# Optimization experiments

Hardware: AMD Instinct MI355X
Metric: run time of the kernel (lower is better)

Reference implementation:

```python
import jax, jax.numpy as jnp
import numpy as np

EPS = 1e-5

def _layer_norm(x, g, b):
    mu = jnp.mean(x, axis=-1, keepdims=True)
    var = jnp.mean(jnp.square(x - mu), axis=-1, keepdims=True)
    return (x - mu) * jax.lax.rsqrt(var + EPS) * g + b

def setup_inputs() -> dict:
    key = jax.random.key(0)
    ks = jax.random.split(key, 8)
    B, S, H, NH, FF = 2, 2048, 2048, 16, 8192
    x = jax.random.normal(ks[0], (B, S, H), dtype=jnp.float32)
    # causal mask: True = masked (matches masked_fill semantics)
    mask = jnp.triu(jnp.ones((S, S), dtype=bool), k=1)
    sc = 0.02
    wq = jax.random.normal(ks[1], (H, H), dtype=jnp.float32) * sc
    wk = jax.random.normal(ks[2], (H, H), dtype=jnp.float32) * sc
    wv = jax.random.normal(ks[3], (H, H), dtype=jnp.float32) * sc
    wo = jax.random.normal(ks[4], (H, H), dtype=jnp.float32) * sc
    w_in = jax.random.normal(ks[5], (H, FF), dtype=jnp.float32) * sc
    w_out = jax.random.normal(ks[6], (FF, H), dtype=jnp.float32) * sc
    ln1_g = jnp.ones((H,), jnp.float32); ln1_b = jnp.zeros((H,), jnp.float32)
    ln2_g = jnp.ones((H,), jnp.float32); ln2_b = jnp.zeros((H,), jnp.float32)
    return {"x": x, "mask": mask, "wq": wq, "wk": wk, "wv": wv, "wo": wo,
            "w_in": w_in, "w_out": w_out,
            "ln1_g": ln1_g, "ln1_b": ln1_b, "ln2_g": ln2_g, "ln2_b": ln2_b}

def reference(x, mask, wq, wk, wv, wo, w_in, w_out, ln1_g, ln1_b, ln2_g, ln2_b):
    B, S, H = x.shape
    NH = 16
    HD = H // NH
    scale = HD ** (-0.5)
    # attention with pre-norm
    xn = _layer_norm(x, ln1_g, ln1_b)
    q = (xn @ wq).reshape(B, S, NH, HD)
    k = (xn @ wk).reshape(B, S, NH, HD)
    v = (xn @ wv).reshape(B, S, NH, HD)
    scores = jnp.einsum('bqhd,bkhd->bhqk', q, k) * scale
    scores = jnp.where(mask[:S, :S], -jnp.inf, scores)
    attn = jax.nn.softmax(scores, axis=-1)
    out = jnp.einsum('bhqk,bkhd->bqhd', attn, v).reshape(B, S, H)
    h = x + out @ wo
    # FFN with pre-norm, tanh-approx GELU
    hn = _layer_norm(h, ln2_g, ln2_b)
    ff = jax.nn.gelu(hn @ w_in, approximate=True) @ w_out
    return h + ff
```

## Files before the change

### kernel.cpp

```cpp
#include <hip/hip_runtime.h>
#include <hip/hip_bf16.h>

#define B_ 2
#define S_ 2048
#define H_ 2048
#define NH_ 16
#define HD_ 128
#define FF_ 8192

typedef __attribute__((ext_vector_type(8))) short bf16x8;
typedef __attribute__((ext_vector_type(4))) float f32x4;

#define NEG_BIG (-1e30f)

#define GLL16(gp, lp)                                                                    \
  __builtin_amdgcn_global_load_lds((const __attribute__((address_space(1))) void*)(gp),  \
                                   (__attribute__((address_space(3))) void*)(lp), 16, 0, 0)

__device__ __forceinline__ float b2f(unsigned short u) {
  union { unsigned int i; float f; } c; c.i = ((unsigned int)u) << 16; return c.f;
}
__device__ __forceinline__ unsigned short f2b(float f) {
  unsigned int u = __float_as_uint(f);
  u += 0x7fffu + ((u >> 16) & 1u);
  return (unsigned short)(u >> 16);
}
__device__ __forceinline__ float ldf(const void* p, size_t i, int f32) {
  return f32 ? ((const float*)p)[i] : b2f(((const unsigned short*)p)[i]);
}
__device__ __forceinline__ void unpack8(uint4 r, float* f) {
  f[0] = b2f((unsigned short)(r.x & 0xffffu)); f[1] = b2f((unsigned short)(r.x >> 16));
  f[2] = b2f((unsigned short)(r.y & 0xffffu)); f[3] = b2f((unsigned short)(r.y >> 16));
  f[4] = b2f((unsigned short)(r.z & 0xffffu)); f[5] = b2f((unsigned short)(r.z >> 16));
  f[6] = b2f((unsigned short)(r.w & 0xffffu)); f[7] = b2f((unsigned short)(r.w >> 16));
}

__global__ void detect_k(const unsigned int* __restrict__ x, int* __restrict__ flagp) {
  if (threadIdx.x == 0) {
    int c = 0;
    for (int i = 0; i < 256; ++i) {
      unsigned int e = (x[i] >> 7) & 0xffu;
      c += (e >= 97u && e <= 130u) ? 1 : 0;
    }
    *flagp = (c < 128) ? 1 : 0;
  }
}

__global__ __launch_bounds__(256) void transpose_k(const void* __restrict__ in,
                                                   unsigned short* __restrict__ out,
                                                   int R, int C,
                                                   const int* __restrict__ flagp) {
  __shared__ unsigned short tile[32][33];
  int f32 = *flagp;
  int r0 = blockIdx.y * 32, c0 = blockIdx.x * 32;
  int tx = threadIdx.x & 31, ty = threadIdx.x >> 5;
#pragma unroll
  for (int p = 0; p < 4; ++p)
    tile[ty + p * 8][tx] = f2b(ldf(in, (size_t)(r0 + ty + p * 8) * C + c0 + tx, f32));
  __syncthreads();
#pragma unroll
  for (int p = 0; p < 4; ++p)
    out[(size_t)(c0 + ty + p * 8) * R + r0 + tx] = tile[tx][ty + p * 8];
}

__global__ __launch_bounds__(256) void v_transpose_k(const unsigned short* __restrict__ qkv,
                                                     unsigned short* __restrict__ VT) {
  __shared__ unsigned short tile[32][33];
  int bh = blockIdx.z;
  int b = bh >> 4, h = bh & 15;
  int s0 = blockIdx.x * 32, d0 = blockIdx.y * 32;
  int tx = threadIdx.x & 31, ty = threadIdx.x >> 5;
#pragma unroll
  for (int p = 0; p < 4; ++p) {
    int s = s0 + ty + p * 8;
    tile[ty + p * 8][tx] = qkv[(size_t)(b * S_ + s) * (3 * H_) + 2 * H_ + h * HD_ + d0 + tx];
  }
  __syncthreads();
#pragma unroll
  for (int p = 0; p < 4; ++p)
    VT[((size_t)bh * HD_ + d0 + ty + p * 8) * S_ + s0 + tx] = tile[tx][ty + p * 8];
}

__global__ __launch_bounds__(256) void ln_k(const void* __restrict__ x,
                                            const void* __restrict__ g,
                                            const void* __restrict__ b,
                                            unsigned short* __restrict__ y,
                                            const int* __restrict__ flagp, int in_mode) {
  __shared__ float red[2][4];
  int f32 = *flagp;
  int xf = in_mode ? f32 : 0;
  int row = blockIdx.x;
  int t = threadIdx.x;
  float v[8];
  size_t base = (size_t)row * H_ + t * 8;
  if (xf) {
    const float4* p = reinterpret_cast<const float4*>((const float*)x + base);
    float4 u0 = p[0], u1 = p[1];
    v[0] = u0.x; v[1] = u0.y; v[2] = u0.z; v[3] = u0.w;
    v[4] = u1.x; v[5] = u1.y; v[6] = u1.z; v[7] = u1.w;
  } else {
    unpack8(*reinterpret_cast<const uint4*>((const unsigned short*)x + base), v);
  }
  float s1 = 0.f, s2 = 0.f;
#pragma unroll
  for (int i = 0; i < 8; ++i) { s1 += v[i]; s2 += v[i] * v[i]; }
#pragma unroll
  for (int off = 32; off > 0; off >>= 1) {
    s1 += __shfl_down(s1, off);
    s2 += __shfl_down(s2, off);
  }
  int w = t >> 6, lane = t & 63;
  if (lane == 0) { red[0][w] = s1; red[1][w] = s2; }
  __syncthreads();
  s1 = red[0][0] + red[0][1] + red[0][2] + red[0][3];
  s2 = red[1][0] + red[1][1] + red[1][2] + red[1][3];
  float mu = s1 * (1.0f / H_);
  float var = s2 * (1.0f / H_) - mu * mu;
  float rinv = rsqrtf(var + 1e-5f);
  float gv[8], bv[8];
#pragma unroll
  for (int i = 0; i < 8; ++i) {
    gv[i] = ldf(g, t * 8 + i, f32);
    bv[i] = ldf(b, t * 8 + i, f32);
  }
  unsigned int o[4];
#pragma unroll
  for (int i = 0; i < 4; ++i) {
    unsigned short lo = f2b((v[2 * i] - mu) * rinv * gv[2 * i] + bv[2 * i]);
    unsigned short hi = f2b((v[2 * i + 1] - mu) * rinv * gv[2 * i + 1] + bv[2 * i + 1]);
    o[i] = (unsigned int)lo | ((unsigned int)hi << 16);
  }
  uint4 ov; ov.x = o[0]; ov.y = o[1]; ov.z = o[2]; ov.w = o[3];
  *reinterpret_cast<uint4*>(y + base) = ov;
}

#define PH_BAR() do { asm volatile("" ::: "memory"); __builtin_amdgcn_s_barrier(); \
                      asm volatile("" ::: "memory"); } while (0)
#define VMC(n) asm volatile("s_waitcnt vmcnt(" #n ")" ::: "memory")

#define STA(buf_, h_, kt_) do {                                                        \
  GLL16(pA0 + (size_t)(h_) * 128 * K + (kt_) * 64, &LdsA[buf_][(h_) * 8192 + lw]);     \
  GLL16(pA1 + (size_t)(h_) * 128 * K + (kt_) * 64, &LdsA[buf_][(h_) * 8192 + 4096 + lw]); } while (0)
#define STB(buf_, h_, kt_) do {                                                        \
  GLL16(pB0 + (size_t)(h_) * 128 * K + (kt_) * 64, &LdsB[buf_][(h_) * 8192 + lw]);     \
  GLL16(pB1 + (size_t)(h_) * 128 * K + (kt_) * 64, &LdsB[buf_][(h_) * 8192 + 4096 + lw]); } while (0)

#define LDA4(AF, buf_, mb_) do { _Pragma("unroll")                                     \
  for (int mi_ = 0; mi_ < 4; ++mi_) {                                                  \
    const unsigned short* _p = &LdsA[buf_][(wr * 128 + ((mb_) + mi_) * 16 + l15) * 64];\
    AF[mi_][0] = *reinterpret_cast<const bf16x8*>(_p + cs0);                           \
    AF[mi_][1] = *reinterpret_cast<const bf16x8*>(_p + cs1); } } while (0)
#define LDB2(BF, buf_, nb_) do { _Pragma("unroll")                                     \
  for (int ni_ = 0; ni_ < 2; ++ni_) {                                                  \
    const unsigned short* _p = &LdsB[buf_][(wc * 64 + ((nb_) + ni_) * 16 + l15) * 64]; \
    BF[ni_][0] = *reinterpret_cast<const bf16x8*>(_p + cs0);                           \
    BF[ni_][1] = *reinterpret_cast<const bf16x8*>(_p + cs1); } } while (0)

#define MF8(AF, BF, MO, NO) do { _Pragma("unroll")                                     \
  for (int mi_ = 0; mi_ < 4; ++mi_) { _Pragma("unroll")                                \
    for (int ni_ = 0; ni_ < 2; ++ni_) {                                                \
      acc[(MO) + mi_][(NO) + ni_] = __builtin_amdgcn_mfma_f32_16x16x32_bf16(           \
          AF[mi_][0], BF[ni_][0], acc[(MO) + mi_][(NO) + ni_], 0, 0, 0);               \
      acc[(MO) + mi_][(NO) + ni_] = __builtin_amdgcn_mfma_f32_16x16x32_bf16(           \
          AF[mi_][1], BF[ni_][1], acc[(MO) + mi_][(NO) + ni_], 0, 0, 0);               \
    } } } while (0)

#define GITER(LAST, tO, tE2, tO2) do {                                                 \
                                                                              \
  LDA4(aL, 0, 0); LDB2(bL, 0, 0);                                                      \
  STA(1, 1, tO);                                                                       \
  PH_BAR(); __builtin_amdgcn_s_setprio(1);                                             \
  MF8(aL, bL, 0, 0);                                                                   \
  __builtin_amdgcn_s_setprio(0);                                                       \
                                                                              \
  LDB2(bH, 0, 2);                                                                      \
  PH_BAR(); __builtin_amdgcn_s_setprio(1);                                             \
  MF8(aL, bH, 0, 2);                                                                   \
  __builtin_amdgcn_s_setprio(0);                                                       \
                                                                              \
  LDA4(aH, 0, 4);                                                                      \
  if (!(LAST)) STB(0, 0, tE2);                                                         \
  PH_BAR(); __builtin_amdgcn_s_setprio(1);                                             \
  MF8(aH, bL, 4, 0);                                                                   \
  __builtin_amdgcn_s_setprio(0);                                                       \
                                                                              \
  if (!(LAST)) { STB(0, 1, tE2); STA(0, 0, tE2); VMC(6); } else { VMC(0); }            \
  PH_BAR(); __builtin_amdgcn_s_setprio(1);                                             \
  MF8(aH, bH, 4, 2);                                                                   \
  __builtin_amdgcn_s_setprio(0);                                                       \
                                                                              \
  LDA4(aL, 1, 0); LDB2(bL, 1, 0);                                                      \
  if (!(LAST)) STA(0, 1, tE2);                                                         \
  PH_BAR(); __builtin_amdgcn_s_setprio(1);                                             \
  MF8(aL, bL, 0, 0);                                                                   \
  __builtin_amdgcn_s_setprio(0);                                                       \
                                                                              \
  LDB2(bH, 1, 2);                                                                      \
  PH_BAR(); __builtin_amdgcn_s_setprio(1);                                             \
  MF8(aL, bH, 0, 2);                                                                   \
  __builtin_amdgcn_s_setprio(0);                                                       \
                                                                              \
  LDA4(aH, 1, 4);                                                                      \
  if (!(LAST)) STB(1, 0, tO2);                                                         \
  PH_BAR(); __builtin_amdgcn_s_setprio(1);                                             \
  MF8(aH, bL, 4, 0);                                                                   \
  __builtin_amdgcn_s_setprio(0);                                                       \
                                                                              \
  if (!(LAST)) { STB(1, 1, tO2); STA(1, 0, tO2); VMC(6); }                             \
  PH_BAR(); __builtin_amdgcn_s_setprio(1);                                             \
  MF8(aH, bH, 4, 2);                                                                   \
  __builtin_amdgcn_s_setprio(0);                                                       \
} while (0)

template <int EPI>
__global__ __launch_bounds__(512) void gemm256(const unsigned short* __restrict__ A,
                                               const unsigned short* __restrict__ BT,
                                               void* __restrict__ C,
                                               const void* __restrict__ resid,
                                               int M, int N, int K,
                                               const int* __restrict__ flagp,
                                               int resid_mode, int store_mode, int nbx,
                                               int nxy, int Klen,
                                               size_t pslice, int prow) {
  (void)M;
  __shared__ unsigned short LdsA[2][16384];
  __shared__ unsigned short LdsB[2][16384];

  unsigned nwg = gridDim.x, q = nwg >> 3;
  unsigned o = blockIdx.x;
  unsigned wg = (o & 7u) * q + (o >> 3);
  int ks = 0;
  if (nxy) { ks = (int)(wg / (unsigned)nxy); wg -= (unsigned)ks * (unsigned)nxy; }
  int bx = (int)(wg % (unsigned)nbx), by = (int)(wg / (unsigned)nbx);
  int m_base = by * 256, n_base = bx * 256;
  size_t koff = (size_t)ks * (size_t)Klen;

  int tid = threadIdx.x;
  int w = tid >> 6, lane = tid & 63;
  int l15 = lane & 15, quad = lane >> 4;
  int wr = w >> 2, wc = w & 3;

  int row0 = w * 8 + (lane >> 3);
  int scb  = (lane & 7) ^ (lane >> 3);
  const unsigned short* pA0 = A + (size_t)(m_base + row0) * K + koff + scb * 8;
  const unsigned short* pA1 = pA0 + (size_t)64 * K;
  const unsigned short* pB0 = BT + (size_t)(n_base + row0) * K + koff + scb * 8;
  const unsigned short* pB1 = pB0 + (size_t)64 * K;
  unsigned lw = (unsigned)w * 512;

  int cs0 = ((quad) ^ (l15 & 7)) * 8;
  int cs1 = ((4 + quad) ^ (l15 & 7)) * 8;

  f32x4 acc[8][4];
#pragma unroll
  for (int i = 0; i < 8; ++i)
#pragma unroll
    for (int j = 0; j < 4; ++j) acc[i][j] = (f32x4){0.f, 0.f, 0.f, 0.f};

  bf16x8 aL[4][2], aH[4][2], bL[2][2], bH[2][2];

  STA(0, 0, 0); STA(0, 1, 0); STB(0, 0, 0); STB(0, 1, 0);
  STB(1, 0, 1); STB(1, 1, 1); STA(1, 0, 1);
  VMC(6);
  PH_BAR();

  int niter = Klen >> 7;
  for (int i = 0; i < niter - 1; ++i) GITER(0, 2 * i + 1, 2 * i + 2, 2 * i + 3);
  GITER(1, 2 * niter - 1, 0, 0);

  int f32 = 0, rf = 0, sf = 0;
  if (EPI != 3) {
    f32 = *flagp;
    rf = resid_mode ? f32 : 0;
    sf = store_mode ? f32 : 0;
  }
#pragma unroll
  for (int mi = 0; mi < 8; ++mi) {
#pragma unroll
    for (int ni = 0; ni < 4; ++ni) {
#pragma unroll
      for (int r = 0; r < 4; ++r) {
        int row = m_base + wr * 128 + mi * 16 + quad * 4 + r;
        int col = n_base + wc * 64 + ni * 16 + l15;
        float v = acc[mi][ni][r];
        if (EPI == 3) {
          ((float*)C)[(size_t)ks * pslice + (size_t)row * prow + col] = v;
        } else {
          size_t idx = (size_t)row * N + col;
          if (EPI == 1) v += ldf(resid, idx, rf);
          if (EPI == 2) {
            float u = v;
            float tt = 0.7978845608028654f * (u + 0.044715f * u * u * u);
            tt = fminf(tt, 15.0f);
            float s = __expf(2.0f * tt);
            v = u * s / (s + 1.0f);
          }
          if (sf) ((float*)C)[idx] = v;
          else    ((unsigned short*)C)[idx] = f2b(v);
        }
      }
    }
  }
}

__global__ __launch_bounds__(256) void red_k(const float* __restrict__ P,
                                             void* __restrict__ out,
                                             const void* __restrict__ resid,
                                             int prow, size_t pslice,
                                             const int* __restrict__ flagp,
                                             int resid_mode, int store_mode) {
  int f32 = *flagp;
  int rf = resid_mode ? f32 : 0;
  int sf = store_mode ? f32 : 0;
  size_t gid = (size_t)blockIdx.x * 256 + threadIdx.x;
  int r = (int)(gid >> 8);
  int c = ((int)gid & 255) * 8;
  size_t pb = (size_t)r * prow + c;
  const float4* p0 = reinterpret_cast<const float4*>(P + pb);
  const float4* p1 = reinterpret_cast<const float4*>(P + pslice + pb);
  float4 a0 = p0[0], a1 = p0[1];
  float4 b0 = p1[0], b1 = p1[1];
  float v[8] = {a0.x + b0.x, a0.y + b0.y, a0.z + b0.z, a0.w + b0.w,
                a1.x + b1.x, a1.y + b1.y, a1.z + b1.z, a1.w + b1.w};
  size_t ob = (size_t)r * 2048 + c;
  if (rf) {
    const float4* rp = reinterpret_cast<const float4*>((const float*)resid + ob);
    float4 r0 = rp[0], r1 = rp[1];
    v[0] += r0.x; v[1] += r0.y; v[2] += r0.z; v[3] += r0.w;
    v[4] += r1.x; v[5] += r1.y; v[6] += r1.z; v[7] += r1.w;
  } else {
    float rr[8];
    unpack8(*reinterpret_cast<const uint4*>((const unsigned short*)resid + ob), rr);
#pragma unroll
    for (int j = 0; j < 8; ++j) v[j] += rr[j];
  }
  if (sf) {
    float4 s0 = {v[0], v[1], v[2], v[3]}, s1 = {v[4], v[5], v[6], v[7]};
    float4* op = reinterpret_cast<float4*>((float*)out + ob);
    op[0] = s0; op[1] = s1;
  } else {
    unsigned int oo[4];
#pragma unroll
    for (int i = 0; i < 4; ++i)
      oo[i] = (unsigned int)f2b(v[2 * i]) | ((unsigned int)f2b(v[2 * i + 1]) << 16);
    uint4 ov; ov.x = oo[0]; ov.y = oo[1]; ov.z = oo[2]; ov.w = oo[3];
    *reinterpret_cast<uint4*>((unsigned short*)out + ob) = ov;
  }
}

__global__ __launch_bounds__(256) void attn_k(const unsigned short* __restrict__ qkv,
                                              const unsigned short* __restrict__ VT,
                                              unsigned short* __restrict__ out) {
  __shared__ unsigned short Ks[2][64 * 128];
  __shared__ unsigned short Vs[2][128 * 64];
  __shared__ unsigned short Ps[4][16][72];
  unsigned o = blockIdx.x;
  int xcd = (int)(o & 7u), j = (int)(o >> 3);
  int bh = xcd + 8 * (j >> 5);
  int qb = 31 - (j & 31);
  int b = bh >> 4, h = bh & 15;
  int q0 = qb * 64;
  int tid = threadIdx.x;
  int w = tid >> 6, lane = tid & 63, l15 = lane & 15, quad = lane >> 4;
  const float scale = 0.08838834764831845f;

  bf16x8 aq[4];
  {
    const unsigned short* qrow =
        qkv + (size_t)(b * S_ + q0 + w * 16 + l15) * (3 * H_) + h * HD_;
#pragma unroll
    for (int ks = 0; ks < 4; ++ks)
      aq[ks] = *reinterpret_cast<const bf16x8*>(qrow + ks * 32 + quad * 8);
  }

  int krow_off = lane >> 4;
  int kcb = lane & 15;
  int vrow_off = lane >> 3;
  int vcb = lane & 7;

  f32x4 o_[8];
#pragma unroll
  for (int f = 0; f < 8; ++f) o_[f] = (f32x4){0.f, 0.f, 0.f, 0.f};
  float m_i[4], l_i[4];
#pragma unroll
  for (int r = 0; r < 4; ++r) { m_i[r] = NEG_BIG; l_i[r] = 0.f; }

  const unsigned short* kbase = qkv + (size_t)b * S_ * (3 * H_) + H_ + h * HD_;
  const unsigned short* vbase = VT + (size_t)bh * HD_ * S_;

#define ATTN_STAGE(buf_, kv0_) do {                                                     \
  _Pragma("unroll")                                                                     \
  for (int t = 0; t < 4; ++t) {                                                         \
    int krow = w * 16 + t * 4 + krow_off;                                               \
    int ksz = kcb ^ (krow & 7);                                                         \
    GLL16(kbase + (size_t)((kv0_) + krow) * (3 * H_) + ksz * 8,                         \
          &Ks[buf_][(w * 16 + t * 4) * 128]);                                           \
    int vrow = w * 32 + t * 8 + vrow_off;                                               \
    int vsz = vcb ^ (vrow & 7);                                                         \
    GLL16(vbase + (size_t)vrow * S_ + (kv0_) + vsz * 8,                                 \
          &Vs[buf_][(w * 32 + t * 8) * 64]);                                            \
  } } while (0)

  ATTN_STAGE(0, 0);
  __syncthreads();

  int cur = 0;
  for (int kv0 = 0; kv0 <= q0; kv0 += 64, cur ^= 1) {
    if (kv0 + 64 <= q0) ATTN_STAGE(cur ^ 1, kv0 + 64);

    f32x4 sc[4];
#pragma unroll
    for (int jj = 0; jj < 4; ++jj) sc[jj] = (f32x4){0.f, 0.f, 0.f, 0.f};
#pragma unroll
    for (int ks = 0; ks < 4; ++ks) {
#pragma unroll
      for (int jj = 0; jj < 4; ++jj) {
        int r = jj * 16 + l15;
        bf16x8 bk = *reinterpret_cast<const bf16x8*>(
            &Ks[cur][r * 128 + (((ks * 4 + quad) ^ (l15 & 7))) * 8]);
        sc[jj] = __builtin_amdgcn_mfma_f32_16x16x32_bf16(aq[ks], bk, sc[jj], 0, 0, 0);
      }
    }
    bool diag = (kv0 == q0);
#pragma unroll
    for (int jj = 0; jj < 4; ++jj)
#pragma unroll
      for (int r = 0; r < 4; ++r) {
        float s = sc[jj][r] * scale;
        if (diag && (jj * 16 + l15 > w * 16 + quad * 4 + r)) s = NEG_BIG;
        sc[jj][r] = s;
      }

    float mx[4];
#pragma unroll
    for (int r = 0; r < 4; ++r) {
      mx[r] = sc[0][r];
#pragma unroll
      for (int jj = 1; jj < 4; ++jj) mx[r] = fmaxf(mx[r], sc[jj][r]);
    }
#pragma unroll
    for (int mm = 1; mm <= 8; mm <<= 1)
#pragma unroll
      for (int r = 0; r < 4; ++r) mx[r] = fmaxf(mx[r], __shfl_xor(mx[r], mm));
    float alpha[4];
#pragma unroll
    for (int r = 0; r < 4; ++r) {
      float mn = fmaxf(m_i[r], mx[r]);
      alpha[r] = __expf(m_i[r] - mn);
      m_i[r] = mn;
    }
    float pr[4][4], rs[4] = {0.f, 0.f, 0.f, 0.f};
#pragma unroll
    for (int jj = 0; jj < 4; ++jj)
#pragma unroll
      for (int r = 0; r < 4; ++r) {
        float p = __expf(sc[jj][r] - m_i[r]);
        pr[jj][r] = p;
        rs[r] += p;
      }
#pragma unroll
    for (int mm = 1; mm <= 8; mm <<= 1)
#pragma unroll
      for (int r = 0; r < 4; ++r) rs[r] += __shfl_xor(rs[r], mm);
#pragma unroll
    for (int r = 0; r < 4; ++r) l_i[r] = l_i[r] * alpha[r] + rs[r];
#pragma unroll
    for (int f = 0; f < 8; ++f)
#pragma unroll
      for (int r = 0; r < 4; ++r) o_[f][r] *= alpha[r];

#pragma unroll
    for (int jj = 0; jj < 4; ++jj)
#pragma unroll
      for (int r = 0; r < 4; ++r)
        Ps[w][quad * 4 + r][jj * 16 + l15] = f2b(pr[jj][r]);

#pragma unroll
    for (int ks2 = 0; ks2 < 2; ++ks2) {
      bf16x8 ap = *reinterpret_cast<const bf16x8*>(&Ps[w][l15][ks2 * 32 + quad * 8]);
#pragma unroll
      for (int f = 0; f < 8; ++f) {
        int r = f * 16 + l15;
        bf16x8 bv = *reinterpret_cast<const bf16x8*>(
            &Vs[cur][r * 64 + (((ks2 * 4 + quad) ^ (l15 & 7))) * 8]);
        o_[f] = __builtin_amdgcn_mfma_f32_16x16x32_bf16(ap, bv, o_[f], 0, 0, 0);
      }
    }

    __syncthreads();
  }

  float inv[4];
#pragma unroll
  for (int r = 0; r < 4; ++r) inv[r] = 1.0f / l_i[r];
#pragma unroll
  for (int f = 0; f < 8; ++f)
#pragma unroll
    for (int r = 0; r < 4; ++r)
      out[(size_t)(b * S_ + q0 + w * 16 + quad * 4 + r) * H_ + h * HD_ + f * 16 + l15] =
          f2b(o_[f][r] * inv[r]);
}

extern "C" void kernel_launch(void* const* d_in, const int* in_sizes, int n_in,
                              void* d_out, int out_size, void* d_ws, size_t ws_size,
                              hipStream_t stream) {
  (void)in_sizes; (void)n_in; (void)out_size; (void)ws_size;
  const void* x     = d_in[0];
  const void* wq    = d_in[2];
  const void* wk    = d_in[3];
  const void* wv    = d_in[4];
  const void* wo    = d_in[5];
  const void* w_in  = d_in[6];
  const void* w_out = d_in[7];
  const void* g1    = d_in[8];
  const void* b1    = d_in[9];
  const void* g2    = d_in[10];
  const void* b2    = d_in[11];
  char* ws = (char*)d_ws;

  const size_t MB = 1024 * 1024;
  unsigned short* W  = (unsigned short*)(ws + 0 * MB);
  unsigned short* E  = (unsigned short*)(ws + 32 * MB);
  unsigned short* F  = (unsigned short*)(ws + 48 * MB);
  unsigned short* Hb = (unsigned short*)(ws + 112 * MB);
  int* flagp         = (int*)(ws + 128 * MB);

  unsigned short* wqkvT = W;
  unsigned short* xn    = E;
  unsigned short* qkv   = F;
  unsigned short* VT    = F + (size_t)B_ * S_ * 3 * H_;
  unsigned short* attnb = E;
  unsigned short* hbuf  = Hb;
  unsigned short* hn    = E;
  unsigned short* ff1   = F;
  float*          Pop   = (float*)F;

  dim3 blk(256);
  dim3 gblk(512);
  detect_k<<<1, 64, 0, stream>>>((const unsigned int*)x, flagp);
  transpose_k<<<dim3(H_ / 32, H_ / 32), blk, 0, stream>>>(wq, wqkvT, H_, H_, flagp);
  transpose_k<<<dim3(H_ / 32, H_ / 32), blk, 0, stream>>>(wk, wqkvT + (size_t)H_ * H_, H_, H_, flagp);
  transpose_k<<<dim3(H_ / 32, H_ / 32), blk, 0, stream>>>(wv, wqkvT + (size_t)2 * H_ * H_, H_, H_, flagp);
  ln_k<<<B_ * S_, blk, 0, stream>>>(x, g1, b1, xn, flagp, 1);
  gemm256<0><<<dim3((3 * H_ / 256) * (B_ * S_ / 256)), gblk, 0, stream>>>(
      xn, wqkvT, qkv, nullptr, B_ * S_, 3 * H_, H_, flagp, 0, 0, 3 * H_ / 256,
      0, H_, 0, 0);
  v_transpose_k<<<dim3(S_ / 32, HD_ / 32, B_ * NH_), blk, 0, stream>>>(qkv, VT);
  attn_k<<<dim3(S_ / 64 * B_ * NH_), blk, 0, stream>>>(qkv, VT, attnb);
  transpose_k<<<dim3(H_ / 32, H_ / 32), blk, 0, stream>>>(wo, W, H_, H_, flagp);
  gemm256<3><<<dim3(2 * (H_ / 256) * (B_ * S_ / 256)), gblk, 0, stream>>>(
      attnb, W, (void*)Pop, nullptr, B_ * S_, H_, H_, flagp, 0, 0, H_ / 256,
      (H_ / 256) * (B_ * S_ / 256), H_ / 2, (size_t)B_ * S_ * H_, H_);
  red_k<<<dim3((B_ * S_ * H_) / (256 * 8)), blk, 0, stream>>>(
      Pop, hbuf, x, H_, (size_t)B_ * S_ * H_, flagp, 1, 0);
  ln_k<<<B_ * S_, blk, 0, stream>>>(hbuf, g2, b2, hn, flagp, 0);
  transpose_k<<<dim3(FF_ / 32, H_ / 32), blk, 0, stream>>>(w_in, W, H_, FF_, flagp);
  gemm256<2><<<dim3((FF_ / 256) * (B_ * S_ / 256)), gblk, 0, stream>>>(
      hn, W, ff1, nullptr, B_ * S_, FF_, H_, flagp, 0, 0, FF_ / 256,
      0, H_, 0, 0);
  transpose_k<<<dim3(H_ / 32, FF_ / 32), blk, 0, stream>>>(w_out, W, FF_, H_, flagp);
  gemm256<3><<<dim3(2 * (H_ / 256) * (B_ * S_ / 256)), gblk, 0, stream>>>(
      ff1, W, (void*)ff1, nullptr, B_ * S_, H_, FF_, flagp, 0, 0, H_ / 256,
      (H_ / 256) * (B_ * S_ / 256), FF_ / 2, (size_t)H_, 2 * H_);
  red_k<<<dim3((B_ * S_ * H_) / (256 * 8)), blk, 0, stream>>>(
      (const float*)ff1, d_out, hbuf, 2 * H_, (size_t)H_, flagp, 0, 1);
}
```

Measured before the change: 920.0 us.

## Add trailing barrier and LDS wait per MFMA phase; group tiles by row

Each MFMA phase now waits for all outstanding LDS reads (lgkmcnt 0) after the barrier and adds a second barrier at its end, making the 8-phase ping-pong schedule stricter. The workgroup-to-tile mapping is also changed so that eight consecutive workgroups share a column block and cover eight adjacent row blocks, aiming for better L2 reuse of the B operand. The extra barriers double synchronisation per iteration and may reduce overlap. The new mapping assumes the row-block count is a multiple of eight.

```diff
diff --git a/kernel.cpp b/kernel.cpp
--- a/kernel.cpp
+++ b/kernel.cpp
@@ -137,6 +137,7 @@
 #define PH_BAR() do { asm volatile("" ::: "memory"); __builtin_amdgcn_s_barrier(); \
                       asm volatile("" ::: "memory"); } while (0)
 #define VMC(n) asm volatile("s_waitcnt vmcnt(" #n ")" ::: "memory")
+#define LGKM0() asm volatile("s_waitcnt lgkmcnt(0)" ::: "memory")
 
 #define STA(buf_, h_, kt_) do {                                                        \
   GLL16(pA0 + (size_t)(h_) * 128 * K + (kt_) * 64, &LdsA[buf_][(h_) * 8192 + lw]);     \
@@ -165,51 +166,40 @@
           AF[mi_][1], BF[ni_][1], acc[(MO) + mi_][(NO) + ni_], 0, 0, 0);               \
     } } } while (0)
 
+#define PH_MFMA(AF, BF, MO, NO) do {                                                   \
+  PH_BAR(); LGKM0(); __builtin_amdgcn_s_setprio(1);                                    \
+  MF8(AF, BF, MO, NO);                                                                 \
+  __builtin_amdgcn_s_setprio(0); PH_BAR(); } while (0)
+
 #define GITER(LAST, tO, tE2, tO2) do {                                                 \
                                                                               \
   LDA4(aL, 0, 0); LDB2(bL, 0, 0);                                                      \
   STA(1, 1, tO);                                                                       \
-  PH_BAR(); __builtin_amdgcn_s_setprio(1);                                             \
-  MF8(aL, bL, 0, 0);                                                                   \
-  __builtin_amdgcn_s_setprio(0);                                                       \
+  PH_MFMA(aL, bL, 0, 0);                                                               \
                                                                               \
   LDB2(bH, 0, 2);                                                                      \
-  PH_BAR(); __builtin_amdgcn_s_setprio(1);                                             \
-  MF8(aL, bH, 0, 2);                                                                   \
-  __builtin_amdgcn_s_setprio(0);                                                       \
+  PH_MFMA(aL, bH, 0, 2);                                                               \
                                                                               \
   LDA4(aH, 0, 4);                                                                      \
   if (!(LAST)) STB(0, 0, tE2);                                                         \
-  PH_BAR(); __builtin_amdgcn_s_setprio(1);                                             \
-  MF8(aH, bL, 4, 0);                                                                   \
-  __builtin_amdgcn_s_setprio(0);                                                       \
+  PH_MFMA(aH, bL, 4, 0);                                                               \
                                                                               \
   if (!(LAST)) { STB(0, 1, tE2); STA(0, 0, tE2); VMC(6); } else { VMC(0); }            \
-  PH_BAR(); __builtin_amdgcn_s_setprio(1);                                             \
-  MF8(aH, bH, 4, 2);                                                                   \
-  __builtin_amdgcn_s_setprio(0);                                                       \
+  PH_MFMA(aH, bH, 4, 2);                                                               \
                                                                               \
   LDA4(aL, 1, 0); LDB2(bL, 1, 0);                                                      \
   if (!(LAST)) STA(0, 1, tE2);                                                         \
-  PH_BAR(); __builtin_amdgcn_s_setprio(1);                                             \
-  MF8(aL, bL, 0, 0);                                                                   \
-  __builtin_amdgcn_s_setprio(0);                                                       \
+  PH_MFMA(aL, bL, 0, 0);                                                               \
                                                                               \
   LDB2(bH, 1, 2);                                                                      \
-  PH_BAR(); __builtin_amdgcn_s_setprio(1);                                             \
-  MF8(aL, bH, 0, 2);                                                                   \
-  __builtin_amdgcn_s_setprio(0);                                                       \
+  PH_MFMA(aL, bH, 0, 2);                                                               \
                                                                               \
   LDA4(aH, 1, 4);                                                                      \
   if (!(LAST)) STB(1, 0, tO2);                                                         \
-  PH_BAR(); __builtin_amdgcn_s_setprio(1);                                             \
-  MF8(aH, bL, 4, 0);                                                                   \
-  __builtin_amdgcn_s_setprio(0);                                                       \
+  PH_MFMA(aH, bL, 4, 0);                                                               \
                                                                               \
   if (!(LAST)) { STB(1, 1, tO2); STA(1, 0, tO2); VMC(6); }                             \
-  PH_BAR(); __builtin_amdgcn_s_setprio(1);                                             \
-  MF8(aH, bH, 4, 2);                                                                   \
-  __builtin_amdgcn_s_setprio(0);                                                       \
+  PH_MFMA(aH, bH, 4, 2);                                                               \
 } while (0)
 
 template <int EPI>
@@ -231,7 +221,8 @@
   unsigned wg = (o & 7u) * q + (o >> 3);
   int ks = 0;
   if (nxy) { ks = (int)(wg / (unsigned)nxy); wg -= (unsigned)ks * (unsigned)nxy; }
-  int bx = (int)(wg % (unsigned)nbx), by = (int)(wg / (unsigned)nbx);
+  int bx = (int)((wg >> 3) % (unsigned)nbx);
+  int by = (int)((wg >> 3) / (unsigned)nbx) * 8 + (int)(wg & 7u);
   int m_base = by * 256, n_base = bx * 256;
   size_t koff = (size_t)ks * (size_t)Klen;
 
```

After: 961.7 us. 1.05x slower.
